# Optimization experiments

Measured on AMD Instinct MI355X. Metric: run time of the kernel, lower is better.

## Reference

```python
import jax, jax.numpy as jnp
import numpy as np
from jax import lax

WINDOW_SIZE = 11
SIGMA = 1.5
C1 = 0.01 ** 2
C2 = 0.03 ** 2


def _gaussian_window(size, sigma):
    coords = np.arange(size, dtype=np.float32) - size // 2
    g = np.exp(-coords ** 2 / (2.0 * sigma ** 2)).astype(np.float32)
    g = g / g.sum()
    w = np.outer(g, g)  # [size, size]
    return jnp.asarray(w)


def _depthwise_conv(x, window2d):
    # x: [B, C, H, W]; window2d: [k, k]
    C = x.shape[1]
    k = window2d.shape[0]
    kernel = jnp.broadcast_to(window2d[None, None], (C, 1, k, k)).astype(x.dtype)
    pad = k // 2
    return lax.conv_general_dilated(
        x, kernel,
        window_strides=(1, 1),
        padding=[(pad, pad), (pad, pad)],
        dimension_numbers=('NCHW', 'OIHW', 'NCHW'),
        feature_group_count=C,
    )


def setup_inputs() -> dict:
    key = jax.random.key(0)
    k1, k2 = jax.random.split(key)
    shape = (32, 3, 512, 512)
    pred = jax.random.uniform(k1, shape, dtype=jnp.float32)
    target = jax.random.uniform(k2, shape, dtype=jnp.float32)
    return {"pred": pred, "target": target}


def reference(pred, target):
    window = _gaussian_window(WINDOW_SIZE, SIGMA)
    mu1 = _depthwise_conv(pred, window)
    mu2 = _depthwise_conv(target, window)
    mu1_sq = mu1 * mu1
    mu2_sq = mu2 * mu2
    mu1_mu2 = mu1 * mu2
    sigma1_sq = _depthwise_conv(pred * pred, window) - mu1_sq
    sigma2_sq = _depthwise_conv(target * target, window) - mu2_sq
    sigma12 = _depthwise_conv(pred * target, window) - mu1_mu2
    ssim_map = ((2.0 * mu1_mu2 + C1) * (2.0 * sigma12 + C2)) / (
        (mu1_sq + mu2_sq + C1) * (sigma1_sq + sigma2_sq + C2))
    return 1.0 - ssim_map.mean()
```

## Files before the change

kernel.cpp:

```cpp
#include <hip/hip_runtime.h>


typedef float f32x2 __attribute__((ext_vector_type(2)));

#define IH 512
#define IW 512
#define TH 8
#define TW 256
#define PW 266
#define RRN 18
#define LPW 268
#define HTILES 64
#define NBLK 12288
#define CPX 1536
#define NPIX 25165824.0f
#define NTHR 512

constexpr float GW[11] = {
    0.00102838f, 0.00759877f, 0.03600078f, 0.10936070f, 0.21300554f,
    0.26601173f,
    0.21300554f, 0.10936070f, 0.03600078f, 0.00759877f, 0.00102838f
};
constexpr float C1f = 0.0001f;
constexpr float C2f = 0.0009f;

__global__ __launch_bounds__(1024) void ssim_reduce(
    const float* __restrict__ ws, float* __restrict__ out)
{
    __shared__ float wsum[16];
    const int tid = threadIdx.x;
    const float4* w4 = reinterpret_cast<const float4*>(ws);
    float s = 0.0f;
    #pragma unroll
    for (int i = 0; i < 3; ++i) {
        const float4 v = w4[tid + i * 1024];
        s += (v.x + v.y) + (v.z + v.w);
    }
    #pragma unroll
    for (int off = 32; off > 0; off >>= 1) s += __shfl_down(s, off, 64);
    if ((tid & 63) == 0) wsum[tid >> 6] = s;
    __syncthreads();
    if (tid == 0) {
        float t = 0.f;
        #pragma unroll
        for (int i = 0; i < 16; ++i) t += wsum[i];
        out[0] = 1.0f - t * (1.0f / NPIX);
    }
}

__global__ __launch_bounds__(NTHR, 8) void ssim_main(
    const float* __restrict__ pred,
    const float* __restrict__ targ,
    float* __restrict__ ws)
{
    __shared__ __align__(16) f32x2 lds01[TH][LPW];
    __shared__ __align__(16) f32x2 lds23[TH][LPW];
    __shared__ float wsum[8];

    const int tid = threadIdx.x;

    const int b  = blockIdx.x;
    const int tl = (b & 7) * CPX + (b >> 3);
    const int ht = tl & (HTILES - 1);
    const int wt = (tl >> 6) & 1;
    const int bc = tl >> 7;

    const int rbase = ht * TH - 5;
    const bool vint = (ht != 0) && (ht != HTILES - 1);
    const float* __restrict__ P = pred + (size_t)bc * (IH * IW);
    const float* __restrict__ T = targ + (size_t)bc * (IH * IW);

    if (tid < PW) {
        const int w = wt * TW - 5 + tid;
        const float wm = ((unsigned)w < (unsigned)IW) ? 1.0f : 0.0f;
        const int wc = w < 0 ? 0 : (w > IW - 1 ? IW - 1 : w);

        float pv[RRN], tv[RRN];
        if (vint) {
            const float* __restrict__ Pp = P + (size_t)rbase * IW + wc;
            const float* __restrict__ Tp = T + (size_t)rbase * IW + wc;
            #pragma unroll
            for (int rr = 0; rr < RRN; ++rr) pv[rr] = Pp[(size_t)rr * IW];
            #pragma unroll
            for (int rr = 0; rr < RRN; ++rr) tv[rr] = Tp[(size_t)rr * IW];
        } else {
            #pragma unroll
            for (int rr = 0; rr < RRN; ++rr) {
                const int h = rbase + rr;
                const int hc = h < 0 ? 0 : (h > IH - 1 ? IH - 1 : h);
                const float rmk = ((unsigned)h < (unsigned)IH) ? 1.0f : 0.0f;
                pv[rr] = P[(size_t)hc * IW + wc] * rmk;
                tv[rr] = T[(size_t)hc * IW + wc] * rmk;
            }
        }
        __builtin_amdgcn_sched_barrier(0);

        f32x2 a01[TH], a23[TH];
        #pragma unroll
        for (int ro = 0; ro < TH; ++ro) {
            a01[ro] = (f32x2){0.f, 0.f};
            a23[ro] = (f32x2){0.f, 0.f};
        }

        #pragma unroll
        for (int rr = 0; rr < RRN; ++rr) {
            const float p = pv[rr], t = tv[rr];
            f32x2 s01; s01.x = p; s01.y = t;
            f32x2 s23;
            s23.x = fmaf(p, p, t * t);
            s23.y = p * t;
            #pragma unroll
            for (int ro = 0; ro < TH; ++ro) {
                const int k = rr - ro;
                if (k >= 0 && k < 11) {
                    const f32x2 g = {GW[k], GW[k]};
                    a01[ro] = __builtin_elementwise_fma(g, s01, a01[ro]);
                    a23[ro] = __builtin_elementwise_fma(g, s23, a23[ro]);
                }
            }
        }
        const f32x2 wmv = {wm, wm};
        #pragma unroll
        for (int ro = 0; ro < TH; ++ro) {
            lds01[ro][tid] = a01[ro] * wmv;
            lds23[ro][tid] = a23[ro] * wmv;
        }
    }
    __syncthreads();

    float lsum = 0.0f;
    {
        const int r  = tid >> 6;
        const int c0 = (tid & 63) << 2;

        float4 u4[7], v4[7];
        const float4* b01 = reinterpret_cast<const float4*>(&lds01[r][c0]);
        const float4* b23 = reinterpret_cast<const float4*>(&lds23[r][c0]);
        #pragma unroll
        for (int q = 0; q < 7; ++q) { u4[q] = b01[q]; v4[q] = b23[q]; }
        const f32x2* x01 = reinterpret_cast<const f32x2*>(u4);
        const f32x2* x23 = reinterpret_cast<const f32x2*>(v4);

        #pragma unroll
        for (int j = 0; j < 4; ++j) {
            f32x2 acc01 = {0.f, 0.f};
            f32x2 acc23 = {0.f, 0.f};
            #pragma unroll
            for (int k = 0; k < 11; ++k) {
                const f32x2 g = {GW[k], GW[k]};
                acc01 = __builtin_elementwise_fma(g, x01[j + k], acc01);
                acc23 = __builtin_elementwise_fma(g, x23[j + k], acc23);
            }
            const float m1  = acc01.x;
            const float m2  = acc01.y;
            const float sPP = acc23.x;
            const float e12 = acc23.y;
            const float m1m2 = m1 * m2;
            const float msq  = fmaf(m1, m1, m2 * m2);
            const float num = fmaf(2.0f, m1m2, C1f) * fmaf(2.0f, (e12 - m1m2), C2f);
            const float den = (msq + C1f) * ((sPP - msq) + C2f);
            lsum = fmaf(num, __builtin_amdgcn_rcpf(den), lsum);
        }
    }

    #pragma unroll
    for (int off = 32; off > 0; off >>= 1) lsum += __shfl_down(lsum, off, 64);
    const int lane = tid & 63;
    const int wv   = tid >> 6;
    if (lane == 0) wsum[wv] = lsum;
    __syncthreads();
    if (tid == 0) {
        float bs = 0.f;
        #pragma unroll
        for (int i = 0; i < 8; ++i) bs += wsum[i];
        ws[b] = bs;
    }
}

extern "C" void kernel_launch(void* const* d_in, const int* in_sizes, int n_in,
                              void* d_out, int out_size, void* d_ws, size_t ws_size,
                              hipStream_t stream) {
    const float* pred = (const float*)d_in[0];
    const float* targ = (const float*)d_in[1];
    float* out = (float*)d_out;
    float* wsf = (float*)d_ws;

    hipLaunchKernelGGL(ssim_main, dim3(NBLK), dim3(NTHR), 0, stream,
                       pred, targ, wsf);
    hipLaunchKernelGGL(ssim_reduce, dim3(1), dim3(1024), 0, stream, wsf, out);
}
```

Baseline: 78.76 us.

## Split vertical conv pass across two thread groups of four output rows each

The block grows from 512 to 640 threads so the vertical Gaussian pass is done by two groups of 320 threads, each loading 14 input rows and producing 4 output rows instead of one group loading 18 rows for 8 outputs. This doubles parallelism in the first phase and lowers the per-thread register footprint, shortening its latency. In exchange each group re-reads 10 halo rows, so global loads per block rise, and the launch bounds drop from 8 to 3 blocks per CU. Idle threads in the horizontal phase also increase because only 512 of the 640 threads take part.

```diff
diff --git a/kernel.cpp b/kernel.cpp
--- a/kernel.cpp
+++ b/kernel.cpp
@@ -8,13 +8,13 @@
 #define TH 8
 #define TW 256
 #define PW 266
-#define RRN 18
+#define GRR 14
 #define LPW 268
 #define HTILES 64
 #define NBLK 12288
 #define CPX 1536
 #define NPIX 25165824.0f
-#define NTHR 512
+#define NTHR 640
 
 constexpr float GW[11] = {
     0.00102838f, 0.00759877f, 0.03600078f, 0.10936070f, 0.21300554f,
@@ -48,14 +48,14 @@
     }
 }
 
-__global__ __launch_bounds__(NTHR, 8) void ssim_main(
+__global__ __launch_bounds__(NTHR, 3) void ssim_main(
     const float* __restrict__ pred,
     const float* __restrict__ targ,
     float* __restrict__ ws)
 {
     __shared__ __align__(16) f32x2 lds01[TH][LPW];
     __shared__ __align__(16) f32x2 lds23[TH][LPW];
-    __shared__ float wsum[8];
+    __shared__ float wsum[10];
 
     const int tid = threadIdx.x;
 
@@ -70,23 +70,27 @@
     const float* __restrict__ P = pred + (size_t)bc * (IH * IW);
     const float* __restrict__ T = targ + (size_t)bc * (IH * IW);
 
-    if (tid < PW) {
-        const int w = wt * TW - 5 + tid;
+    const int grp  = tid / 320;
+    const int lane = tid - grp * 320;
+    const int gbase = rbase + grp * 4;
+
+    if (lane < PW) {
+        const int w = wt * TW - 5 + lane;
         const float wm = ((unsigned)w < (unsigned)IW) ? 1.0f : 0.0f;
         const int wc = w < 0 ? 0 : (w > IW - 1 ? IW - 1 : w);
 
-        float pv[RRN], tv[RRN];
+        float pv[GRR], tv[GRR];
         if (vint) {
-            const float* __restrict__ Pp = P + (size_t)rbase * IW + wc;
-            const float* __restrict__ Tp = T + (size_t)rbase * IW + wc;
+            const float* __restrict__ Pp = P + (size_t)gbase * IW + wc;
+            const float* __restrict__ Tp = T + (size_t)gbase * IW + wc;
             #pragma unroll
-            for (int rr = 0; rr < RRN; ++rr) pv[rr] = Pp[(size_t)rr * IW];
+            for (int rr = 0; rr < GRR; ++rr) pv[rr] = Pp[(size_t)rr * IW];
             #pragma unroll
-            for (int rr = 0; rr < RRN; ++rr) tv[rr] = Tp[(size_t)rr * IW];
+            for (int rr = 0; rr < GRR; ++rr) tv[rr] = Tp[(size_t)rr * IW];
         } else {
             #pragma unroll
-            for (int rr = 0; rr < RRN; ++rr) {
-                const int h = rbase + rr;
+            for (int rr = 0; rr < GRR; ++rr) {
+                const int h = gbase + rr;
                 const int hc = h < 0 ? 0 : (h > IH - 1 ? IH - 1 : h);
                 const float rmk = ((unsigned)h < (unsigned)IH) ? 1.0f : 0.0f;
                 pv[rr] = P[(size_t)hc * IW + wc] * rmk;
@@ -95,41 +99,42 @@
         }
         __builtin_amdgcn_sched_barrier(0);
 
-        f32x2 a01[TH], a23[TH];
+        f32x2 a01[4], a23[4];
         #pragma unroll
-        for (int ro = 0; ro < TH; ++ro) {
-            a01[ro] = (f32x2){0.f, 0.f};
-            a23[ro] = (f32x2){0.f, 0.f};
+        for (int q = 0; q < 4; ++q) {
+            a01[q] = (f32x2){0.f, 0.f};
+            a23[q] = (f32x2){0.f, 0.f};
         }
 
         #pragma unroll
-        for (int rr = 0; rr < RRN; ++rr) {
+        for (int rr = 0; rr < GRR; ++rr) {
             const float p = pv[rr], t = tv[rr];
             f32x2 s01; s01.x = p; s01.y = t;
             f32x2 s23;
             s23.x = fmaf(p, p, t * t);
             s23.y = p * t;
             #pragma unroll
-            for (int ro = 0; ro < TH; ++ro) {
-                const int k = rr - ro;
+            for (int q = 0; q < 4; ++q) {
+                const int k = rr - q;
                 if (k >= 0 && k < 11) {
                     const f32x2 g = {GW[k], GW[k]};
-                    a01[ro] = __builtin_elementwise_fma(g, s01, a01[ro]);
-                    a23[ro] = __builtin_elementwise_fma(g, s23, a23[ro]);
+                    a01[q] = __builtin_elementwise_fma(g, s01, a01[q]);
+                    a23[q] = __builtin_elementwise_fma(g, s23, a23[q]);
                 }
             }
         }
         const f32x2 wmv = {wm, wm};
         #pragma unroll
-        for (int ro = 0; ro < TH; ++ro) {
-            lds01[ro][tid] = a01[ro] * wmv;
-            lds23[ro][tid] = a23[ro] * wmv;
+        for (int q = 0; q < 4; ++q) {
+            const int ro = grp * 4 + q;
+            lds01[ro][lane] = a01[q] * wmv;
+            lds23[ro][lane] = a23[q] * wmv;
         }
     }
     __syncthreads();
 
     float lsum = 0.0f;
-    {
+    if (tid < 512) {
         const int r  = tid >> 6;
         const int c0 = (tid & 63) << 2;
 
@@ -165,14 +170,14 @@
 
     #pragma unroll
     for (int off = 32; off > 0; off >>= 1) lsum += __shfl_down(lsum, off, 64);
-    const int lane = tid & 63;
-    const int wv   = tid >> 6;
-    if (lane == 0) wsum[wv] = lsum;
+    const int wl = tid & 63;
+    const int wv = tid >> 6;
+    if (wl == 0) wsum[wv] = lsum;
     __syncthreads();
     if (tid == 0) {
         float bs = 0.f;
         #pragma unroll
-        for (int i = 0; i < 8; ++i) bs += wsum[i];
+        for (int i = 0; i < 10; ++i) bs += wsum[i];
         ws[b] = bs;
     }
 }
```

Result: slower. 95.12 us (+20.8%).

## Switch to full-width 4-row tiles with zero-padded LDS halos

Applied to the files above, without the earlier changes.

Reshapes each block's tile from 8 rows by 256 columns to 4 rows by the full 512-column width. Every thread now loads a column without horizontal halo clamping or masking, and the horizontal padding is written as explicit zeros in LDS. This removes the 10-column horizontal halo reloads and leaves no idle threads in the vertical pass. The trade-off is that the vertical halo overhead grows, from 18 loaded rows per 8 output rows to 14 rows per 4.

```diff
diff --git a/kernel.cpp b/kernel.cpp
--- a/kernel.cpp
+++ b/kernel.cpp
@@ -5,12 +5,11 @@
 
 #define IH 512
 #define IW 512
-#define TH 8
-#define TW 256
-#define PW 266
-#define RRN 18
-#define LPW 268
-#define HTILES 64
+#define TH 4
+#define TW 512
+#define RRN 14
+#define LPW 524
+#define HTILES 128
 #define NBLK 12288
 #define CPX 1536
 #define NPIX 25165824.0f
@@ -62,18 +61,15 @@
     const int b  = blockIdx.x;
     const int tl = (b & 7) * CPX + (b >> 3);
     const int ht = tl & (HTILES - 1);
-    const int wt = (tl >> 6) & 1;
     const int bc = tl >> 7;
 
     const int rbase = ht * TH - 5;
-    const bool vint = (ht != 0) && (ht != HTILES - 1);
+    const bool vint = (rbase >= 0) && (rbase + RRN <= IH);
     const float* __restrict__ P = pred + (size_t)bc * (IH * IW);
     const float* __restrict__ T = targ + (size_t)bc * (IH * IW);
 
-    if (tid < PW) {
-        const int w = wt * TW - 5 + tid;
-        const float wm = ((unsigned)w < (unsigned)IW) ? 1.0f : 0.0f;
-        const int wc = w < 0 ? 0 : (w > IW - 1 ? IW - 1 : w);
+    {
+        const int wc = tid;
 
         float pv[RRN], tv[RRN];
         if (vint) {
@@ -97,9 +93,9 @@
 
         f32x2 a01[TH], a23[TH];
         #pragma unroll
-        for (int ro = 0; ro < TH; ++ro) {
-            a01[ro] = (f32x2){0.f, 0.f};
-            a23[ro] = (f32x2){0.f, 0.f};
+        for (int q = 0; q < TH; ++q) {
+            a01[q] = (f32x2){0.f, 0.f};
+            a23[q] = (f32x2){0.f, 0.f};
         }
 
         #pragma unroll
@@ -110,28 +106,36 @@
             s23.x = fmaf(p, p, t * t);
             s23.y = p * t;
             #pragma unroll
-            for (int ro = 0; ro < TH; ++ro) {
-                const int k = rr - ro;
+            for (int q = 0; q < TH; ++q) {
+                const int k = rr - q;
                 if (k >= 0 && k < 11) {
                     const f32x2 g = {GW[k], GW[k]};
-                    a01[ro] = __builtin_elementwise_fma(g, s01, a01[ro]);
-                    a23[ro] = __builtin_elementwise_fma(g, s23, a23[ro]);
+                    a01[q] = __builtin_elementwise_fma(g, s01, a01[q]);
+                    a23[q] = __builtin_elementwise_fma(g, s23, a23[q]);
                 }
             }
         }
-        const f32x2 wmv = {wm, wm};
         #pragma unroll
-        for (int ro = 0; ro < TH; ++ro) {
-            lds01[ro][tid] = a01[ro] * wmv;
-            lds23[ro][tid] = a23[ro] * wmv;
+        for (int q = 0; q < TH; ++q) {
+            lds01[q][tid + 5] = a01[q];
+            lds23[q][tid + 5] = a23[q];
+        }
+        if (tid < 10) {
+            const int pi = (tid < 5) ? tid : (512 + tid);
+            const f32x2 z = {0.f, 0.f};
+            #pragma unroll
+            for (int q = 0; q < TH; ++q) {
+                lds01[q][pi] = z;
+                lds23[q][pi] = z;
+            }
         }
     }
     __syncthreads();
 
     float lsum = 0.0f;
     {
-        const int r  = tid >> 6;
-        const int c0 = (tid & 63) << 2;
+        const int r  = tid >> 7;
+        const int c0 = (tid & 127) << 2;
 
         float4 u4[7], v4[7];
         const float4* b01 = reinterpret_cast<const float4*>(&lds01[r][c0]);
```

Measured after the change: 79.26 us. No clear change (+0.6%).
